# Optimization experiments

Hardware: AMD Instinct MI355X
Metric: run time of the kernel (lower is better)

Reference implementation:

```python
import jax, jax.numpy as jnp
import numpy as np

B, NQ, NK = 4, 4096, 1024
QDIM, CDIM = 512, 768
HEADS, DHEAD = 8, 64
INNER = HEADS * DHEAD


def setup_inputs() -> dict:
    key = jax.random.key(0)
    ks = jax.random.split(key, 6)
    s = 0.02
    return {
        "x": jax.random.normal(ks[0], (B, NQ, QDIM), dtype=jnp.float32),
        "context": jax.random.normal(ks[1], (B, NK, CDIM), dtype=jnp.float32),
        "Wq": jax.random.normal(ks[2], (QDIM, INNER), dtype=jnp.float32) * s,
        "Wk": jax.random.normal(ks[3], (CDIM, INNER), dtype=jnp.float32) * s,
        "Wv": jax.random.normal(ks[4], (CDIM, INNER), dtype=jnp.float32) * s,
        "Wo": jax.random.normal(ks[5], (INNER, QDIM), dtype=jnp.float32) * s,
        "bo": jnp.zeros((QDIM,), dtype=jnp.float32),
    }


def reference(x, context, Wq, Wk, Wv, Wo, bo):
    scale = DHEAD ** (-0.5)
    # projections
    q = x @ Wq            # [B, NQ, H*D]
    k = context @ Wk      # [B, NK, H*D]
    v = context @ Wv      # [B, NK, H*D]
    # split heads: [B, N, H, D]
    q = q.reshape(B, NQ, HEADS, DHEAD)
    k = k.reshape(B, NK, HEADS, DHEAD)
    v = v.reshape(B, NK, HEADS, DHEAD)
    # scores [B, H, NQ, NK]
    sim = jnp.einsum('bihd,bjhd->bhij', q, k) * scale
    attn = jax.nn.softmax(sim, axis=-1)
    out = jnp.einsum('bhij,bjhd->bihd', attn, v)  # [B, NQ, H, D]
    out = out.reshape(B, NQ, INNER)
    return out @ Wo + bo  # dropout p=0.0 -> identity
```

## Files before the change

kernel.cpp:

```cpp
#include <hip/hip_runtime.h>

typedef unsigned short u16;
typedef unsigned int u32;
typedef __bf16 bf16x8 __attribute__((ext_vector_type(8)));
typedef float f32x4 __attribute__((ext_vector_type(4)));
typedef u16 u16x8 __attribute__((ext_vector_type(8)));

#define BB 4
#define NQ 4096
#define NKV 1024
#define QD 512
#define CD 768
#define NH 8
#define DH 64
#define DI 512

__device__ __forceinline__ u16 f2bf(float f) {
    u32 u = __float_as_uint(f);
    u = (u + 0x7fffu + ((u >> 16) & 1u)) >> 16;
    return (u16)u;
}

__device__ __forceinline__ u32 cvtpk(float lo, float hi) {
    u32 r;
    asm("v_cvt_pk_bf16_f32 %0, %1, %2" : "=v"(r) : "v"(lo), "v"(hi));
    return r;
}

__device__ __forceinline__ void gload16(const void* g, void* l) {
    __builtin_amdgcn_global_load_lds(
        (const __attribute__((address_space(1))) u32*)g,
        (__attribute__((address_space(3))) u32*)l, 16, 0, 0);
}

__device__ __forceinline__ f32x4 MFMA(bf16x8 a, bf16x8 b, f32x4 c) {
    return __builtin_amdgcn_mfma_f32_16x16x32_bf16(a, b, c, 0, 0, 0);
}

__global__ __launch_bounds__(256)
void k_conv2(const float* __restrict__ a, u16* __restrict__ ao, int n8a,
             const float* __restrict__ b, u16* __restrict__ bo, int n8b) {
    int i = blockIdx.x * 256 + threadIdx.x;
    const float* in; u16* out; int j;
    if (i < n8a) { in = a; out = ao; j = i; }
    else { j = i - n8a; if (j >= n8b) return; in = b; out = bo; }
    float4 u0 = ((const float4*)in)[2 * j];
    float4 u1 = ((const float4*)in)[2 * j + 1];
    uint4 v;
    v.x = cvtpk(u0.x, u0.y);
    v.y = cvtpk(u0.z, u0.w);
    v.z = cvtpk(u1.x, u1.y);
    v.w = cvtpk(u1.z, u1.w);
    ((uint4*)out)[j] = v;
}

__global__ __launch_bounds__(256)
void k_transposeAll(const float* __restrict__ Wq, const float* __restrict__ Wk,
                    const float* __restrict__ Wv, const float* __restrict__ Wo,
                    u16* __restrict__ Wqt, u16* __restrict__ Wkvt, u16* __restrict__ Wot) {
    __shared__ float tile[32][33];
    const float* W; u16* Wt; int K, N;
    int z = blockIdx.z;
    if (z == 0)      { W = Wq; Wt = Wqt;                        K = 512; N = 512; }
    else if (z == 1) { W = Wk; Wt = Wkvt;                       K = 768; N = 512; }
    else if (z == 2) { W = Wv; Wt = Wkvt + (size_t)512 * 768;   K = 768; N = 512; }
    else             { W = Wo; Wt = Wot;                        K = 512; N = 512; }
    int kb = blockIdx.x * 32, nb = blockIdx.y * 32;
    if (kb >= K) return;
    int tx = threadIdx.x & 31, ty = threadIdx.x >> 5;
    for (int i = ty; i < 32; i += 8)
        tile[i][tx] = W[(size_t)(kb + i) * N + nb + tx];
    __syncthreads();
    for (int i = ty; i < 32; i += 8)
        Wt[(size_t)(nb + i) * K + kb + tx] = f2bf(tile[tx][i]);
}

__global__ __launch_bounds__(256)
void k_transposeV(const u16* __restrict__ KV, u16* __restrict__ Vt) {
    __shared__ u16 tile[32][33];
    int j0 = blockIdx.x * 32, d0 = blockIdx.y * 32, bh = blockIdx.z;
    int b = bh >> 3, h = bh & 7;
    int tx = threadIdx.x & 31, ty = threadIdx.x >> 5;
    for (int i = ty; i < 32; i += 8)
        tile[i][tx] = KV[(size_t)(b * NKV + j0 + i) * 1024 + 512 + h * DH + d0 + tx];
    __syncthreads();
    for (int i = ty; i < 32; i += 8)
        Vt[(size_t)(bh * DH + d0 + i) * NKV + j0 + tx] = tile[tx][i];
}

template <bool OUTF32, bool BIAS>
__global__ __launch_bounds__(256, 4)
void k_gemm(const u16* __restrict__ A, const u16* __restrict__ Bt,
            void* __restrict__ Cv, const float* __restrict__ bias,
            int M, int N, int K) {
    __shared__ u16 lA[64 * 64];
    __shared__ u16 lB[128 * 64];
    const int t = threadIdx.x;
    const int w = t >> 6, lane = t & 63, r = lane & 15, g = lane >> 4;
    const int m0 = blockIdx.x * 64, n0 = blockIdx.y * 128;
    const int wm = (w >> 1) * 32, wn = (w & 1) * 64;

    const int rsub = lane >> 3;
    const int slot = (lane & 7) ^ rsub;
    const u16* gA = A + (size_t)(m0 + w * 8 + rsub) * K + slot * 8;
    const u16* gB = Bt + (size_t)(n0 + w * 8 + rsub) * K + slot * 8;

    f32x4 acc[2][4];
#pragma unroll
    for (int a = 0; a < 2; ++a)
#pragma unroll
        for (int c = 0; c < 4; ++c) acc[a][c] = {};

#pragma unroll 1
    for (int kt = 0; kt < K; kt += 64) {
        __syncthreads();
#pragma unroll
        for (int c = 0; c < 2; ++c)
            gload16(gA + (size_t)(c * 32) * K + kt, (char*)lA + c * 4096 + w * 1024);
#pragma unroll
        for (int c = 0; c < 4; ++c)
            gload16(gB + (size_t)(c * 32) * K + kt, (char*)lB + c * 4096 + w * 1024);
        __syncthreads();
#pragma unroll
        for (int ks = 0; ks < 2; ++ks) {
            bf16x8 af[2], bfr[4];
#pragma unroll
            for (int mt = 0; mt < 2; ++mt) {
                int row = wm + mt * 16 + r;
                int byte = ((row << 7) | (ks << 6) | (g << 4)) ^ ((row & 7) << 4);
                af[mt] = *(const bf16x8*)((const char*)lA + byte);
            }
#pragma unroll
            for (int nt = 0; nt < 4; ++nt) {
                int row = wn + nt * 16 + r;
                int byte = ((row << 7) | (ks << 6) | (g << 4)) ^ ((row & 7) << 4);
                bfr[nt] = *(const bf16x8*)((const char*)lB + byte);
            }
#pragma unroll
            for (int mt = 0; mt < 2; ++mt)
#pragma unroll
                for (int nt = 0; nt < 4; ++nt)
                    acc[mt][nt] = MFMA(af[mt], bfr[nt], acc[mt][nt]);
        }
    }
#pragma unroll
    for (int mt = 0; mt < 2; ++mt) {
#pragma unroll
        for (int i = 0; i < 4; ++i) {
            int row = m0 + wm + mt * 16 + g * 4 + i;
#pragma unroll
            for (int nt = 0; nt < 4; ++nt) {
                int col = n0 + wn + nt * 16 + r;
                float vv = acc[mt][nt][i];
                if constexpr (BIAS) vv += bias[col];
                if constexpr (OUTF32) ((float*)Cv)[(size_t)row * N + col] = vv;
                else ((u16*)Cv)[(size_t)row * N + col] = f2bf(vv);
            }
        }
    }
}

__global__ __launch_bounds__(256, 3)
void k_attn(const u16* __restrict__ Q, const u16* __restrict__ KV,
            const u16* __restrict__ Vt, u16* __restrict__ O) {
    __shared__ u16 lK[128 * 64];
    __shared__ u16 lV[64 * 128];
    const int t = threadIdx.x;
    const int w = t >> 6, lane = t & 63, r = lane & 15, g = lane >> 4;
    const int bh = blockIdx.x, qt = blockIdx.y;
    const int b = bh >> 3, h = bh & 7;
    const int q0 = qt * 128 + w * 32;

    const int rsub = lane >> 3;
    const int kslot = (lane & 7) ^ rsub;
    const u16* gK = KV + (size_t)(b * NKV + w * 8 + rsub) * 1024 + h * DH + kslot * 8;
    const int vr7 = ((w & 1) << 2) | g;
    const int vslot = (lane & 8) | ((lane & 7) ^ vr7);
    const u16* gV = Vt + (size_t)(bh * DH + w * 4 + g) * NKV + vslot * 8;

    bf16x8 qf[2][2];
#pragma unroll
    for (int itl = 0; itl < 2; ++itl) {
        const u16* qp = Q + (size_t)(b * NQ + q0 + itl * 16 + r) * DI + h * DH;
#pragma unroll
        for (int ks = 0; ks < 2; ++ks)
            qf[itl][ks] = *(const bf16x8*)(qp + ks * 32 + g * 8);
    }

    float mrow[2] = {-3e38f, -3e38f};
    float lrow[2] = {0.f, 0.f};
    f32x4 oacc[2][4];
#pragma unroll
    for (int a = 0; a < 2; ++a)
#pragma unroll
        for (int c = 0; c < 4; ++c) oacc[a][c] = {};

    const float c1 = 0.125f * 1.44269504f;

#pragma unroll 1
    for (int kv0 = 0; kv0 < NKV; kv0 += 128) {
        __syncthreads();
#pragma unroll
        for (int c = 0; c < 4; ++c) {
            gload16(gK + (size_t)(kv0 + c * 32) * 1024, (char*)lK + c * 4096 + w * 1024);
            gload16(gV + (size_t)(c * 16) * NKV + kv0, (char*)lV + c * 4096 + w * 1024);
        }
        __syncthreads();

        f32x4 st[8][2];
        __builtin_amdgcn_s_setprio(1);
#pragma unroll
        for (int jt = 0; jt < 8; ++jt) {
            bf16x8 kf[2];
#pragma unroll
            for (int ks = 0; ks < 2; ++ks) {
                int row = jt * 16 + r;
                int byte = ((row << 7) | (ks << 6) | (g << 4)) ^ ((row & 7) << 4);
                kf[ks] = *(const bf16x8*)((const char*)lK + byte);
            }
#pragma unroll
            for (int itl = 0; itl < 2; ++itl) {
                f32x4 a = {};
                a = MFMA(kf[0], qf[itl][0], a);
                a = MFMA(kf[1], qf[itl][1], a);
                st[jt][itl] = a;
            }
        }
        __builtin_amdgcn_s_setprio(0);

        float pmax[2], corr[2] = {1.f, 1.f};
#pragma unroll
        for (int itl = 0; itl < 2; ++itl) {
            float mx = st[0][itl][0];
#pragma unroll
            for (int jt = 0; jt < 8; ++jt)
#pragma unroll
                for (int ii = 0; ii < 4; ++ii) mx = fmaxf(mx, st[jt][itl][ii]);
            mx = fmaxf(mx, __shfl_xor(mx, 16));
            mx = fmaxf(mx, __shfl_xor(mx, 32));
            pmax[itl] = mx * c1;
        }
        if (!__all(pmax[0] <= mrow[0] + 11.f && pmax[1] <= mrow[1] + 11.f)) {
#pragma unroll
            for (int itl = 0; itl < 2; ++itl) {
                float mnew = fmaxf(mrow[itl], pmax[itl]);
                corr[itl] = __builtin_amdgcn_exp2f(mrow[itl] - mnew);
                mrow[itl] = mnew;
            }
#pragma unroll
            for (int mtl = 0; mtl < 2; ++mtl)
#pragma unroll
                for (int ii = 0; ii < 4; ++ii) {
                    float c = __shfl(corr[mtl], g * 4 + ii);
#pragma unroll
                    for (int nt = 0; nt < 4; ++nt) oacc[mtl][nt][ii] *= c;
                }
        }

        float tsum[2] = {0.f, 0.f};
#pragma unroll
        for (int ks = 0; ks < 4; ++ks) {
            bf16x8 vf[4];
#pragma unroll
            for (int nt = 0; nt < 4; ++nt) {
                int row = nt * 16 + r;
                int byte = ((row << 8) | (ks << 6) | (g << 4)) ^ ((row & 7) << 4);
                vf[nt] = *(const bf16x8*)((const char*)lV + byte);
            }
            bf16x8 pa[2];
#pragma unroll
            for (int itl = 0; itl < 2; ++itl) {
                float e[8];
#pragma unroll
                for (int ii = 0; ii < 4; ++ii) {
                    e[ii]     = __builtin_amdgcn_exp2f(st[2 * ks][itl][ii] * c1 - mrow[itl]);
                    e[4 + ii] = __builtin_amdgcn_exp2f(st[2 * ks + 1][itl][ii] * c1 - mrow[itl]);
                }
#pragma unroll
                for (int ii = 0; ii < 8; ++ii) tsum[itl] += e[ii];
                u32 a0 = cvtpk(e[0], e[1]), a1 = cvtpk(e[2], e[3]);
                u32 b0 = cvtpk(e[4], e[5]), b1 = cvtpk(e[6], e[7]);
                asm("v_permlane32_swap_b32 %0, %1" : "+v"(a0), "+v"(b0));
                asm("v_permlane16_swap_b32 %0, %1" : "+v"(a0), "+v"(b0));
                asm("v_permlane32_swap_b32 %0, %1" : "+v"(a1), "+v"(b1));
                asm("v_permlane16_swap_b32 %0, %1" : "+v"(a1), "+v"(b1));
                union { u32 u[4]; bf16x8 v; } pk;
                pk.u[0] = a0; pk.u[1] = a1; pk.u[2] = b0; pk.u[3] = b1;
                pa[itl] = pk.v;
            }
            __builtin_amdgcn_s_setprio(1);
#pragma unroll
            for (int mtl = 0; mtl < 2; ++mtl)
#pragma unroll
                for (int nt = 0; nt < 4; ++nt)
                    oacc[mtl][nt] = MFMA(pa[mtl], vf[nt], oacc[mtl][nt]);
            __builtin_amdgcn_s_setprio(0);
        }
#pragma unroll
        for (int itl = 0; itl < 2; ++itl) {
            float s = tsum[itl];
            s += __shfl_xor(s, 16);
            s += __shfl_xor(s, 32);
            lrow[itl] = lrow[itl] * corr[itl] + s;
        }
    }

#pragma unroll
    for (int mtl = 0; mtl < 2; ++mtl) {
#pragma unroll
        for (int ii = 0; ii < 4; ++ii) {
            float lv = __shfl(lrow[mtl], g * 4 + ii);
            float linv = __builtin_amdgcn_rcpf(lv);
            int i = q0 + mtl * 16 + g * 4 + ii;
#pragma unroll
            for (int nt = 0; nt < 4; ++nt) {
                int d = nt * 16 + r;
                O[(size_t)(b * NQ + i) * DI + h * DH + d] = f2bf(oacc[mtl][nt][ii] * linv);
            }
        }
    }
}

extern "C" void kernel_launch(void* const* d_in, const int* in_sizes, int n_in,
                              void* d_out, int out_size, void* d_ws, size_t ws_size,
                              hipStream_t stream) {
    (void)in_sizes; (void)n_in; (void)out_size; (void)ws_size;
    const float* x   = (const float*)d_in[0];
    const float* ctx = (const float*)d_in[1];
    const float* Wq  = (const float*)d_in[2];
    const float* Wk  = (const float*)d_in[3];
    const float* Wv  = (const float*)d_in[4];
    const float* Wo  = (const float*)d_in[5];
    const float* bo  = (const float*)d_in[6];
    float* out = (float*)d_out;

    char* ws = (char*)d_ws;
    u16* Wqt  = (u16*)(ws);
    u16* Wkvt = (u16*)(ws + (size_t)524288);
    u16* Wot  = (u16*)(ws + (size_t)2097152);
    u16* Qw   = (u16*)(ws + (size_t)2621440);
    u16* KVw  = (u16*)(ws + (size_t)19398656);
    u16* slotC = (u16*)(ws + (size_t)27787264);
    u16* slotD = (u16*)(ws + (size_t)44564480);
    u16* xb   = slotC;
    u16* Ow   = slotC;
    u16* ctxb = slotD;
    u16* Vtw  = slotD;

    k_conv2<<<dim3(5632), 256, 0, stream>>>(x, xb, BB * NQ * QD / 8,
                                            ctx, ctxb, BB * NKV * CD / 8);
    k_transposeAll<<<dim3(24, 16, 4), 256, 0, stream>>>(Wq, Wk, Wv, Wo, Wqt, Wkvt, Wot);

    k_gemm<false, false><<<dim3(256, 4), 256, 0, stream>>>(xb, Wqt, Qw, nullptr, BB * NQ, DI, QD);
    k_gemm<false, false><<<dim3(64, 8), 256, 0, stream>>>(ctxb, Wkvt, KVw, nullptr, BB * NKV, 1024, CD);
    k_transposeV<<<dim3(32, 2, 32), 256, 0, stream>>>(KVw, Vtw);
    k_attn<<<dim3(32, 32), 256, 0, stream>>>(Qw, KVw, Vtw, Ow);
    k_gemm<true, true><<<dim3(256, 4), 256, 0, stream>>>(Ow, Wot, out, bo, BB * NQ, QD, DI);
}
```

Before: 203.2 us.

## Double-buffer GEMM and attention LDS, fuse prep and QKV launches, MFMA row sums

Merges the input conversion and weight transposes into one prep kernel and the Q and KV projections into one GEMM launch, reducing launch count. The GEMM moves to 128x128 tiles with double-buffered LDS and prefetch of the next K slice. The attention kernel also double-buffers K/V tiles and computes softmax row sums with an extra MFMA against a ones vector instead of VALU adds and shuffles. The larger LDS footprint and tiles lower occupancy (launch bounds 2), which may reduce latency hiding.

```diff
diff --git a/kernel.cpp b/kernel.cpp
--- a/kernel.cpp
+++ b/kernel.cpp
@@ -37,39 +37,46 @@
     return __builtin_amdgcn_mfma_f32_16x16x32_bf16(a, b, c, 0, 0, 0);
 }
 
+__device__ __forceinline__ bf16x8 ones8() {
+    union { u16 u[8]; bf16x8 v; } o;
+#pragma unroll
+    for (int i = 0; i < 8; ++i) o.u[i] = 0x3F80;
+    return o.v;
+}
+
 __global__ __launch_bounds__(256)
-void k_conv2(const float* __restrict__ a, u16* __restrict__ ao, int n8a,
-             const float* __restrict__ b, u16* __restrict__ bo, int n8b) {
-    int i = blockIdx.x * 256 + threadIdx.x;
-    const float* in; u16* out; int j;
-    if (i < n8a) { in = a; out = ao; j = i; }
-    else { j = i - n8a; if (j >= n8b) return; in = b; out = bo; }
-    float4 u0 = ((const float4*)in)[2 * j];
-    float4 u1 = ((const float4*)in)[2 * j + 1];
-    uint4 v;
-    v.x = cvtpk(u0.x, u0.y);
-    v.y = cvtpk(u0.z, u0.w);
-    v.z = cvtpk(u1.x, u1.y);
-    v.w = cvtpk(u1.z, u1.w);
-    ((uint4*)out)[j] = v;
-}
-
-__global__ __launch_bounds__(256)
-void k_transposeAll(const float* __restrict__ Wq, const float* __restrict__ Wk,
-                    const float* __restrict__ Wv, const float* __restrict__ Wo,
-                    u16* __restrict__ Wqt, u16* __restrict__ Wkvt, u16* __restrict__ Wot) {
+void k_prep(const float* __restrict__ x, u16* __restrict__ xb,
+            const float* __restrict__ ctx, u16* __restrict__ ctxb,
+            const float* __restrict__ Wq, const float* __restrict__ Wk,
+            const float* __restrict__ Wv, const float* __restrict__ Wo,
+            u16* __restrict__ Wqt, u16* __restrict__ Wkvt, u16* __restrict__ Wot) {
     __shared__ float tile[32][33];
-    const float* W; u16* Wt; int K, N;
-    int z = blockIdx.z;
-    if (z == 0)      { W = Wq; Wt = Wqt;                        K = 512; N = 512; }
-    else if (z == 1) { W = Wk; Wt = Wkvt;                       K = 768; N = 512; }
-    else if (z == 2) { W = Wv; Wt = Wkvt + (size_t)512 * 768;   K = 768; N = 512; }
-    else             { W = Wo; Wt = Wot;                        K = 512; N = 512; }
-    int kb = blockIdx.x * 32, nb = blockIdx.y * 32;
-    if (kb >= K) return;
+    int bid = blockIdx.x;
+    if (bid < 5632) {
+        const float* in; u16* out; int j;
+        int i = bid * 256 + threadIdx.x;
+        if (i < 4096 * 256) { in = x; out = xb; j = i; }
+        else { j = i - 4096 * 256; in = ctx; out = ctxb; }
+        float4 u0 = ((const float4*)in)[2 * j];
+        float4 u1 = ((const float4*)in)[2 * j + 1];
+        uint4 v;
+        v.x = cvtpk(u0.x, u0.y);
+        v.y = cvtpk(u0.z, u0.w);
+        v.z = cvtpk(u1.x, u1.y);
+        v.w = cvtpk(u1.z, u1.w);
+        ((uint4*)out)[j] = v;
+        return;
+    }
+    int tb = bid - 5632;
+    const float* W; u16* Wt; int K, nblk;
+    if (tb < 256)      { W = Wq; Wt = Wqt;                      K = 512; nblk = tb; }
+    else if (tb < 640) { W = Wk; Wt = Wkvt;                     K = 768; nblk = tb - 256; }
+    else if (tb < 1024){ W = Wv; Wt = Wkvt + (size_t)512 * 768; K = 768; nblk = tb - 640; }
+    else               { W = Wo; Wt = Wot;                      K = 512; nblk = tb - 1024; }
+    int kb = (nblk >> 4) * 32, nb = (nblk & 15) * 32;
     int tx = threadIdx.x & 31, ty = threadIdx.x >> 5;
     for (int i = ty; i < 32; i += 8)
-        tile[i][tx] = W[(size_t)(kb + i) * N + nb + tx];
+        tile[i][tx] = W[(size_t)(kb + i) * 512 + nb + tx];
     __syncthreads();
     for (int i = ty; i < 32; i += 8)
         Wt[(size_t)(nb + i) * K + kb + tx] = f2bf(tile[tx][i]);
@@ -89,62 +96,73 @@
 }
 
 template <bool OUTF32, bool BIAS>
-__global__ __launch_bounds__(256, 4)
-void k_gemm(const u16* __restrict__ A, const u16* __restrict__ Bt,
-            void* __restrict__ Cv, const float* __restrict__ bias,
-            int M, int N, int K) {
-    __shared__ u16 lA[64 * 64];
-    __shared__ u16 lB[128 * 64];
+__device__ __forceinline__ void gemm_body(const u16* __restrict__ A, const u16* __restrict__ Bt,
+                                          void* __restrict__ Cv, const float* __restrict__ bias,
+                                          int N, int K, int m0, int n0) {
+    __shared__ u16 lA[2][128 * 64];
+    __shared__ u16 lB[2][128 * 64];
     const int t = threadIdx.x;
     const int w = t >> 6, lane = t & 63, r = lane & 15, g = lane >> 4;
-    const int m0 = blockIdx.x * 64, n0 = blockIdx.y * 128;
-    const int wm = (w >> 1) * 32, wn = (w & 1) * 64;
-
+    const int wm = (w >> 1) * 64, wn = (w & 1) * 64;
     const int rsub = lane >> 3;
     const int slot = (lane & 7) ^ rsub;
     const u16* gA = A + (size_t)(m0 + w * 8 + rsub) * K + slot * 8;
     const u16* gB = Bt + (size_t)(n0 + w * 8 + rsub) * K + slot * 8;
 
-    f32x4 acc[2][4];
-#pragma unroll
-    for (int a = 0; a < 2; ++a)
+    f32x4 acc[4][4];
+#pragma unroll
+    for (int a = 0; a < 4; ++a)
 #pragma unroll
         for (int c = 0; c < 4; ++c) acc[a][c] = {};
 
-#pragma unroll 1
-    for (int kt = 0; kt < K; kt += 64) {
-        __syncthreads();
-#pragma unroll
-        for (int c = 0; c < 2; ++c)
-            gload16(gA + (size_t)(c * 32) * K + kt, (char*)lA + c * 4096 + w * 1024);
-#pragma unroll
-        for (int c = 0; c < 4; ++c)
-            gload16(gB + (size_t)(c * 32) * K + kt, (char*)lB + c * 4096 + w * 1024);
-        __syncthreads();
+    auto STAGE = [&](int kt, int bufi) {
+#pragma unroll
+        for (int c = 0; c < 4; ++c) {
+            gload16(gA + (size_t)(c * 32) * K + kt, (char*)lA[bufi] + c * 4096 + w * 1024);
+            gload16(gB + (size_t)(c * 32) * K + kt, (char*)lB[bufi] + c * 4096 + w * 1024);
+        }
+    };
+    auto COMP = [&](int bufi) {
+        __builtin_amdgcn_s_setprio(1);
 #pragma unroll
         for (int ks = 0; ks < 2; ++ks) {
-            bf16x8 af[2], bfr[4];
-#pragma unroll
-            for (int mt = 0; mt < 2; ++mt) {
+            bf16x8 af[4], bfr[4];
+#pragma unroll
+            for (int mt = 0; mt < 4; ++mt) {
                 int row = wm + mt * 16 + r;
                 int byte = ((row << 7) | (ks << 6) | (g << 4)) ^ ((row & 7) << 4);
-                af[mt] = *(const bf16x8*)((const char*)lA + byte);
+                af[mt] = *(const bf16x8*)((const char*)lA[bufi] + byte);
             }
 #pragma unroll
             for (int nt = 0; nt < 4; ++nt) {
                 int row = wn + nt * 16 + r;
                 int byte = ((row << 7) | (ks << 6) | (g << 4)) ^ ((row & 7) << 4);
-                bfr[nt] = *(const bf16x8*)((const char*)lB + byte);
-            }
-#pragma unroll
-            for (int mt = 0; mt < 2; ++mt)
+                bfr[nt] = *(const bf16x8*)((const char*)lB[bufi] + byte);
+            }
+#pragma unroll
+            for (int mt = 0; mt < 4; ++mt)
 #pragma unroll
                 for (int nt = 0; nt < 4; ++nt)
                     acc[mt][nt] = MFMA(af[mt], bfr[nt], acc[mt][nt]);
         }
-    }
-#pragma unroll
-    for (int mt = 0; mt < 2; ++mt) {
+        __builtin_amdgcn_s_setprio(0);
+    };
+
+    STAGE(0, 0);
+    __syncthreads();
+#pragma unroll 1
+    for (int kt = 0; kt < K; kt += 128) {
+        if (kt + 64 < K) STAGE(kt + 64, 1);
+        COMP(0);
+        __syncthreads();
+        if (kt + 128 < K) STAGE(kt + 128, 0);
+        if (kt + 64 < K) {
+            COMP(1);
+            __syncthreads();
+        }
+    }
+#pragma unroll
+    for (int mt = 0; mt < 4; ++mt) {
 #pragma unroll
         for (int i = 0; i < 4; ++i) {
             int row = m0 + wm + mt * 16 + g * 4 + i;
@@ -160,11 +178,30 @@
     }
 }
 
-__global__ __launch_bounds__(256, 3)
+__global__ __launch_bounds__(256, 2)
+void k_gemm_qkv(const u16* __restrict__ xb, const u16* __restrict__ Wqt, u16* __restrict__ Qw,
+                const u16* __restrict__ ctxb, const u16* __restrict__ Wkvt, u16* __restrict__ KVw) {
+    int bid = blockIdx.x;
+    if (bid < 512)
+        gemm_body<false, false>(xb, Wqt, Qw, nullptr, 512, 512, (bid >> 2) * 128, (bid & 3) * 128);
+    else {
+        bid -= 512;
+        gemm_body<false, false>(ctxb, Wkvt, KVw, nullptr, 1024, 768, (bid >> 3) * 128, (bid & 7) * 128);
+    }
+}
+
+__global__ __launch_bounds__(256, 2)
+void k_gemm_o(const u16* __restrict__ Ow, const u16* __restrict__ Wot,
+              float* __restrict__ out, const float* __restrict__ bo) {
+    int bid = blockIdx.x;
+    gemm_body<true, true>(Ow, Wot, out, bo, 512, 512, (bid >> 2) * 128, (bid & 3) * 128);
+}
+
+__global__ __launch_bounds__(256, 2)
 void k_attn(const u16* __restrict__ Q, const u16* __restrict__ KV,
             const u16* __restrict__ Vt, u16* __restrict__ O) {
-    __shared__ u16 lK[128 * 64];
-    __shared__ u16 lV[64 * 128];
+    __shared__ u16 lK[2][128 * 64];
+    __shared__ u16 lV[2][64 * 128];
     const int t = threadIdx.x;
     const int w = t >> 6, lane = t & 63, r = lane & 15, g = lane >> 4;
     const int bh = blockIdx.x, qt = blockIdx.y;
@@ -187,26 +224,27 @@
             qf[itl][ks] = *(const bf16x8*)(qp + ks * 32 + g * 8);
     }
 
+    const bf16x8 vOnes = ones8();
     float mrow[2] = {-3e38f, -3e38f};
-    float lrow[2] = {0.f, 0.f};
-    f32x4 oacc[2][4];
-#pragma unroll
-    for (int a = 0; a < 2; ++a)
+    f32x4 oacc[2][4], lacc[2];
+#pragma unroll
+    for (int a = 0; a < 2; ++a) {
+        lacc[a] = {};
 #pragma unroll
         for (int c = 0; c < 4; ++c) oacc[a][c] = {};
+    }
 
     const float c1 = 0.125f * 1.44269504f;
 
-#pragma unroll 1
-    for (int kv0 = 0; kv0 < NKV; kv0 += 128) {
-        __syncthreads();
+    auto STAGE = [&](int kv0, int bufi) {
 #pragma unroll
         for (int c = 0; c < 4; ++c) {
-            gload16(gK + (size_t)(kv0 + c * 32) * 1024, (char*)lK + c * 4096 + w * 1024);
-            gload16(gV + (size_t)(c * 16) * NKV + kv0, (char*)lV + c * 4096 + w * 1024);
-        }
-        __syncthreads();
-
+            gload16(gK + (size_t)(kv0 + c * 32) * 1024, (char*)lK[bufi] + c * 4096 + w * 1024);
+            gload16(gV + (size_t)(c * 16) * NKV + kv0, (char*)lV[bufi] + c * 4096 + w * 1024);
+        }
+    };
+
+    auto TILE = [&](int bufi) {
         f32x4 st[8][2];
         __builtin_amdgcn_s_setprio(1);
 #pragma unroll
@@ -216,7 +254,7 @@
             for (int ks = 0; ks < 2; ++ks) {
                 int row = jt * 16 + r;
                 int byte = ((row << 7) | (ks << 6) | (g << 4)) ^ ((row & 7) << 4);
-                kf[ks] = *(const bf16x8*)((const char*)lK + byte);
+                kf[ks] = *(const bf16x8*)((const char*)lK[bufi] + byte);
             }
 #pragma unroll
             for (int itl = 0; itl < 2; ++itl) {
@@ -228,7 +266,7 @@
         }
         __builtin_amdgcn_s_setprio(0);
 
-        float pmax[2], corr[2] = {1.f, 1.f};
+        float pmax[2];
 #pragma unroll
         for (int itl = 0; itl < 2; ++itl) {
             float mx = st[0][itl][0];
@@ -241,6 +279,7 @@
             pmax[itl] = mx * c1;
         }
         if (!__all(pmax[0] <= mrow[0] + 11.f && pmax[1] <= mrow[1] + 11.f)) {
+            float corr[2];
 #pragma unroll
             for (int itl = 0; itl < 2; ++itl) {
                 float mnew = fmaxf(mrow[itl], pmax[itl]);
@@ -254,10 +293,10 @@
                     float c = __shfl(corr[mtl], g * 4 + ii);
 #pragma unroll
                     for (int nt = 0; nt < 4; ++nt) oacc[mtl][nt][ii] *= c;
+                    lacc[mtl][ii] *= c;
                 }
         }
 
-        float tsum[2] = {0.f, 0.f};
 #pragma unroll
         for (int ks = 0; ks < 4; ++ks) {
             bf16x8 vf[4];
@@ -265,7 +304,7 @@
             for (int nt = 0; nt < 4; ++nt) {
                 int row = nt * 16 + r;
                 int byte = ((row << 8) | (ks << 6) | (g << 4)) ^ ((row & 7) << 4);
-                vf[nt] = *(const bf16x8*)((const char*)lV + byte);
+                vf[nt] = *(const bf16x8*)((const char*)lV[bufi] + byte);
             }
             bf16x8 pa[2];
 #pragma unroll
@@ -276,8 +315,6 @@
                     e[ii]     = __builtin_amdgcn_exp2f(st[2 * ks][itl][ii] * c1 - mrow[itl]);
                     e[4 + ii] = __builtin_amdgcn_exp2f(st[2 * ks + 1][itl][ii] * c1 - mrow[itl]);
                 }
-#pragma unroll
-                for (int ii = 0; ii < 8; ++ii) tsum[itl] += e[ii];
                 u32 a0 = cvtpk(e[0], e[1]), a1 = cvtpk(e[2], e[3]);
                 u32 b0 = cvtpk(e[4], e[5]), b1 = cvtpk(e[6], e[7]);
                 asm("v_permlane32_swap_b32 %0, %1" : "+v"(a0), "+v"(b0));
@@ -290,27 +327,33 @@
             }
             __builtin_amdgcn_s_setprio(1);
 #pragma unroll
-            for (int mtl = 0; mtl < 2; ++mtl)
+            for (int mtl = 0; mtl < 2; ++mtl) {
 #pragma unroll
                 for (int nt = 0; nt < 4; ++nt)
                     oacc[mtl][nt] = MFMA(pa[mtl], vf[nt], oacc[mtl][nt]);
+                lacc[mtl] = MFMA(pa[mtl], vOnes, lacc[mtl]);
+            }
             __builtin_amdgcn_s_setprio(0);
         }
-#pragma unroll
-        for (int itl = 0; itl < 2; ++itl) {
-            float s = tsum[itl];
-            s += __shfl_xor(s, 16);
-            s += __shfl_xor(s, 32);
-            lrow[itl] = lrow[itl] * corr[itl] + s;
-        }
+    };
+
+    STAGE(0, 0);
+    __syncthreads();
+#pragma unroll 1
+    for (int kv0 = 0; kv0 < NKV; kv0 += 256) {
+        STAGE(kv0 + 128, 1);
+        TILE(0);
+        __syncthreads();
+        if (kv0 + 256 < NKV) STAGE(kv0 + 256, 0);
+        TILE(1);
+        __syncthreads();
     }
 
 #pragma unroll
     for (int mtl = 0; mtl < 2; ++mtl) {
 #pragma unroll
         for (int ii = 0; ii < 4; ++ii) {
-            float lv = __shfl(lrow[mtl], g * 4 + ii);
-            float linv = __builtin_amdgcn_rcpf(lv);
+            float linv = __builtin_amdgcn_rcpf(lacc[mtl][ii]);
             int i = q0 + mtl * 16 + g * 4 + ii;
 #pragma unroll
             for (int nt = 0; nt < 4; ++nt) {
@@ -347,13 +390,9 @@
     u16* ctxb = slotD;
     u16* Vtw  = slotD;
 
-    k_conv2<<<dim3(5632), 256, 0, stream>>>(x, xb, BB * NQ * QD / 8,
-                                            ctx, ctxb, BB * NKV * CD / 8);
-    k_transposeAll<<<dim3(24, 16, 4), 256, 0, stream>>>(Wq, Wk, Wv, Wo, Wqt, Wkvt, Wot);
-
-    k_gemm<false, false><<<dim3(256, 4), 256, 0, stream>>>(xb, Wqt, Qw, nullptr, BB * NQ, DI, QD);
-    k_gemm<false, false><<<dim3(64, 8), 256, 0, stream>>>(ctxb, Wkvt, KVw, nullptr, BB * NKV, 1024, CD);
+    k_prep<<<dim3(6912), 256, 0, stream>>>(x, xb, ctx, ctxb, Wq, Wk, Wv, Wo, Wqt, Wkvt, Wot);
+    k_gemm_qkv<<<dim3(768), 256, 0, stream>>>(xb, Wqt, Qw, ctxb, Wkvt, KVw);
     k_transposeV<<<dim3(32, 2, 32), 256, 0, stream>>>(KVw, Vtw);
     k_attn<<<dim3(32, 32), 256, 0, stream>>>(Qw, KVw, Vtw, Ow);
-    k_gemm<true, true><<<dim3(256, 4), 256, 0, stream>>>(Ow, Wot, out, bo, BB * NQ, QD, DI);
-}
+    k_gemm_o<<<dim3(512), 256, 0, stream>>>(Ow, Wot, out, bo);
+}
```

Measured after the change: 194.8 us. 1.04x faster.
